# Kernel optimization log

Hardware: AMD Instinct MI355X
Metric: run time of the kernel (lower is better)

The kernel has to match this reference:

```python
import jax, jax.numpy as jnp
import numpy as np

NUM_HEADS = 16
TOP_K = 2

def setup_inputs() -> dict:
    key = jax.random.key(0)
    ks = jax.random.split(key, 5)
    B, D, E = 8192, 2048, 8
    x = jax.random.normal(ks[0], (B, D), dtype=jnp.float32)
    W_qkv = jax.random.normal(ks[1], (E, D, 3 * D), dtype=jnp.float32) * 0.02  # (in,out) per expert
    W_gate = jax.random.normal(ks[2], (D, E), dtype=jnp.float32) * 0.02
    b_gate = jnp.zeros((E,), dtype=jnp.float32)
    W_proj = jax.random.normal(ks[3], (D, D), dtype=jnp.float32) * 0.02
    b_proj = jnp.zeros((D,), dtype=jnp.float32)
    return {"x": x, "W_qkv": W_qkv, "W_gate": W_gate, "b_gate": b_gate,
            "W_proj": W_proj, "b_proj": b_proj}


def reference(x, W_qkv, W_gate, b_gate, W_proj, b_proj):
    B, D = x.shape
    E = W_qkv.shape[0]
    H = NUM_HEADS
    hd = D // H
    scale = float(hd) ** -0.5

    # gating + top-k (sparse gate weights, zeros for non-selected experts)
    gate_scores = jax.nn.softmax(x @ W_gate + b_gate, axis=-1)        # (B, E)
    topk_vals, topk_idx = jax.lax.top_k(gate_scores, TOP_K)           # (B, K)
    gw = jnp.zeros_like(gate_scores).at[jnp.arange(B)[:, None], topk_idx].add(topk_vals)

    # gate-weighted combine of expert QKV projections (linear => combine after GEMM)
    qkv = jnp.zeros((B, 3 * D), dtype=x.dtype)
    for e in range(E):  # fixed small expert count; each iter is one big GEMM
        qkv = qkv + gw[:, e:e + 1] * (x @ W_qkv[e])
    qkv = qkv.reshape(B, 3, H, hd)

    # NOTE: the torch source writes `q = k = v = torch.zeros(...)` then uses
    # in-place `+=`, so q, k, v ALIAS one tensor: all equal gate*(q_i+k_i+v_i).
    # We replicate that exact math faithfully.
    s = qkv.sum(axis=1)                                               # (B, H, hd)

    attn = jax.nn.softmax(jnp.einsum('bhd,bgd->bhg', s, s) * scale, axis=-1)  # (B, H, H)
    out = jnp.einsum('bhg,bgd->bhd', attn, s)                         # (B, H, hd)
    out = out.transpose(0, 2, 1).reshape(B, D)                        # matches .transpose(1,2).reshape
    return out @ W_proj + b_proj
```

## Files before the change

kernel.cpp:

```cpp
#include <hip/hip_runtime.h>

#define B_ROWS 8192
#define DDIM 2048
#define NEXP 8
#define NASSIGN (B_ROWS * 2)
#define MAX_TILES 80

typedef unsigned short u16;
typedef short bf16x8 __attribute__((ext_vector_type(8)));
typedef float f32x4 __attribute__((ext_vector_type(4)));

#define M_CNT 0
#define M_FILL 8
#define M_SEG 16
#define M_CTRA 24
#define M_CTRB 32
#define M_NT 40
#define M_TE 48
#define M_TB 128
#define M_TR 208

__device__ __forceinline__ u16 f2b(float f) {
  union { float f; unsigned u; } c; c.f = f;
  return (u16)((c.u + 0x7fffu + ((c.u >> 16) & 1u)) >> 16);
}
__device__ __forceinline__ float b2f(u16 h) {
  union { unsigned u; float f; } c; c.u = ((unsigned)h) << 16;
  return c.f;
}
__device__ __forceinline__ void async16(u16* lds, const u16* g) {
  __builtin_amdgcn_global_load_lds(
      (const __attribute__((address_space(1))) unsigned int*)g,
      (__attribute__((address_space(3))) unsigned int*)lds, 16, 0, 0);
}

__global__ void init_meta_kernel(int* meta) {
  int t = threadIdx.x;
  if (t < 48) meta[t] = 0;
}

template <int NSUM>
__global__ __launch_bounds__(256) void prep_transpose(
    const float* __restrict__ Win, u16* __restrict__ Wout, int ldin) {
  __shared__ u16 tl[64][72];
  int bx = blockIdx.x;
  int nt = bx & 31, kt = (bx >> 5) & 31, e = bx >> 10;
  int t = threadIdx.x;
  const size_t in_base = (size_t)e * DDIM * (size_t)ldin;
  int k0 = kt * 64, n0 = nt * 64;
#pragma unroll
  for (int i = 0; i < 4; ++i) {
    int idx = i * 256 + t;
    int kl = idx >> 4, f4 = idx & 15;
    const float* p = Win + in_base + (size_t)(k0 + kl) * ldin + n0 + f4 * 4;
    float4 v = *(const float4*)p;
    if (NSUM == 3) {
      float4 v1 = *(const float4*)(p + 2048);
      float4 v2 = *(const float4*)(p + 4096);
      v.x += v1.x + v2.x; v.y += v1.y + v2.y;
      v.z += v1.z + v2.z; v.w += v1.w + v2.w;
    }
    tl[f4 * 4 + 0][kl] = f2b(v.x);
    tl[f4 * 4 + 1][kl] = f2b(v.y);
    tl[f4 * 4 + 2][kl] = f2b(v.z);
    tl[f4 * 4 + 3][kl] = f2b(v.w);
  }
  __syncthreads();
  u16* out = Wout + (size_t)e * DDIM * DDIM;
#pragma unroll
  for (int i = 0; i < 2; ++i) {
    int idx = i * 256 + t;
    int nl = idx >> 3, kc = idx & 7;
    const u16* r = &tl[nl][kc * 8];
    uint4 pk;
    pk.x = (unsigned)r[0] | ((unsigned)r[1] << 16);
    pk.y = (unsigned)r[2] | ((unsigned)r[3] << 16);
    pk.z = (unsigned)r[4] | ((unsigned)r[5] << 16);
    pk.w = (unsigned)r[6] | ((unsigned)r[7] << 16);
    *(uint4*)(out + (size_t)(n0 + nl) * DDIM + k0 + kc * 8) = pk;
  }
}

__global__ __launch_bounds__(256) void gate_kernel(
    const float* __restrict__ x, const float* __restrict__ Wg,
    const float* __restrict__ bg, u16* __restrict__ xb,
    int* __restrict__ e01, float* __restrict__ w01, int* __restrict__ meta) {
  int b = blockIdx.x, t = threadIdx.x;
  const float* xr = x + (size_t)b * DDIM;
  float4 v0 = ((const float4*)xr)[2 * t];
  float4 v1 = ((const float4*)xr)[2 * t + 1];
  float xv[8] = {v0.x, v0.y, v0.z, v0.w, v1.x, v1.y, v1.z, v1.w};
  uint4 pk;
  pk.x = (unsigned)f2b(xv[0]) | ((unsigned)f2b(xv[1]) << 16);
  pk.y = (unsigned)f2b(xv[2]) | ((unsigned)f2b(xv[3]) << 16);
  pk.z = (unsigned)f2b(xv[4]) | ((unsigned)f2b(xv[5]) << 16);
  pk.w = (unsigned)f2b(xv[6]) | ((unsigned)f2b(xv[7]) << 16);
  *(uint4*)(xb + (size_t)b * DDIM + t * 8) = pk;

  double acc[8] = {0, 0, 0, 0, 0, 0, 0, 0};
#pragma unroll
  for (int j = 0; j < 8; ++j) {
    const float4* wr = (const float4*)(Wg + (size_t)(t * 8 + j) * 8);
    float4 wa = wr[0], wb = wr[1];
    double xd = (double)xv[j];
    acc[0] += xd * wa.x; acc[1] += xd * wa.y;
    acc[2] += xd * wa.z; acc[3] += xd * wa.w;
    acc[4] += xd * wb.x; acc[5] += xd * wb.y;
    acc[6] += xd * wb.z; acc[7] += xd * wb.w;
  }
#pragma unroll
  for (int e = 0; e < 8; ++e)
    for (int m2 = 32; m2; m2 >>= 1) acc[e] += __shfl_xor(acc[e], m2);
  __shared__ double red[4][8];
  if ((t & 63) == 0)
    for (int e = 0; e < 8; ++e) red[t >> 6][e] = acc[e];
  __syncthreads();
  if (t == 0) {
    double l[8];
    for (int e = 0; e < 8; ++e)
      l[e] = red[0][e] + red[1][e] + red[2][e] + red[3][e] + (double)bg[e];
    double mx = l[0];
    for (int e = 1; e < 8; ++e) mx = l[e] > mx ? l[e] : mx;
    double p[8], s = 0;
    for (int e = 0; e < 8; ++e) { p[e] = exp(l[e] - mx); s += p[e]; }
    int i1 = 0;
    for (int e = 1; e < 8; ++e) if (p[e] > p[i1]) i1 = e;
    int i2 = (i1 == 0) ? 1 : 0;
    for (int e = 0; e < 8; ++e)
      if (e != i1 && p[e] > p[i2]) i2 = e;
    e01[2 * b] = i1; e01[2 * b + 1] = i2;
    w01[2 * b] = (float)(p[i1] / s);
    w01[2 * b + 1] = (float)(p[i2] / s);
    atomicAdd(&meta[M_CNT + i1], 1);
    atomicAdd(&meta[M_CNT + i2], 1);
  }
}

__global__ void scan_kernel(int* meta) {
  if (threadIdx.x != 0) return;
  int total = 0;
  for (int e = 0; e < 8; ++e) { meta[M_SEG + e] = total; total += meta[M_CNT + e]; }
  int tt = 0;
  for (int e = 0; e < 8; ++e) {
    int cnt = meta[M_CNT + e];
    int ntl = (cnt + 255) >> 8;
    for (int i = 0; i < ntl; ++i) {
      meta[M_TE + tt] = e;
      meta[M_TB + tt] = meta[M_SEG + e] + i * 256;
      meta[M_TR + tt] = cnt - i * 256;
      ++tt;
    }
  }
  meta[M_NT] = tt;
  for (; tt < MAX_TILES; ++tt) { meta[M_TE + tt] = 0; meta[M_TB + tt] = 0; meta[M_TR + tt] = 0; }
}

__global__ __launch_bounds__(256) void build_kernel(
    const int* __restrict__ e01, const float* __restrict__ w01,
    int* __restrict__ meta, int* __restrict__ rows, float* __restrict__ wt,
    int* __restrict__ rowpos) {
  int b = blockIdx.x * 256 + threadIdx.x;
  if (b >= B_ROWS) return;
#pragma unroll
  for (int s = 0; s < 2; ++s) {
    int e = e01[2 * b + s];
    float w = w01[2 * b + s];
    int p = meta[M_SEG + e] + atomicAdd(&meta[M_FILL + e], 1);
    rows[p] = b;
    wt[p] = w;
    rowpos[2 * b + s] = p;
  }
}

#define BAR()                           \
  do {                                  \
    __builtin_amdgcn_sched_barrier(0);  \
    __builtin_amdgcn_s_barrier();       \
    __builtin_amdgcn_sched_barrier(0);  \
  } while (0)
#define VMCNT2() asm volatile("s_waitcnt vmcnt(2)" ::: "memory")
#define VMCNT0() asm volatile("s_waitcnt vmcnt(0)" ::: "memory")
#define LGKM0()                                       \
  do {                                                \
    asm volatile("s_waitcnt lgkmcnt(0)" ::: "memory"); \
    __builtin_amdgcn_sched_barrier(0);                \
  } while (0)

#define STAGE_A(L, T, BB) async16(&lds[BB][0][(L)*4096 + t * 8], srcA[L] + (size_t)(T)*64)
#define STAGE_B(L, T, BB) async16(&lds[BB][1][(L)*4096 + t * 8], srcB[L] + (size_t)(T)*64)

#define READ_A(QM)                                                   \
  do {                                                               \
    _Pragma("unroll") for (int i_ = 0; i_ < 4; ++i_) {               \
      int rb_ = baseA + ((QM)*64 + i_ * 16) * 128;                   \
      af[i_][0] = *(const bf16x8*)(pA + rb_ + ck0);                  \
      af[i_][1] = *(const bf16x8*)(pA + rb_ + ck1);                  \
    }                                                                \
  } while (0)
#define READ_B(H)                                                    \
  do {                                                               \
    _Pragma("unroll") for (int j_ = 0; j_ < 2; ++j_) {               \
      int rb_ = baseB + (((H)*2 + j_) * 16) * 128;                   \
      bfr[(H)*2 + j_][0] = *(const bf16x8*)(pB + rb_ + ck0);         \
      bfr[(H)*2 + j_][1] = *(const bf16x8*)(pB + rb_ + ck1);         \
    }                                                                \
  } while (0)
#define MFMA16(QM, QN)                                                         \
  do {                                                                         \
    _Pragma("unroll") for (int i_ = 0; i_ < 4; ++i_) {                         \
      _Pragma("unroll") for (int j_ = 0; j_ < 2; ++j_) {                       \
        acc[(QM)*4 + i_][(QN)*2 + j_] = __builtin_amdgcn_mfma_f32_16x16x32_bf16( \
            af[i_][0], bfr[(QN)*2 + j_][0], acc[(QM)*4 + i_][(QN)*2 + j_], 0, 0, 0); \
        acc[(QM)*4 + i_][(QN)*2 + j_] = __builtin_amdgcn_mfma_f32_16x16x32_bf16( \
            af[i_][1], bfr[(QN)*2 + j_][1], acc[(QM)*4 + i_][(QN)*2 + j_], 0, 0, 0); \
      }                                                                        \
    }                                                                          \
  } while (0)

template <int MODE>
__global__ __launch_bounds__(512, 2) void gemm256_kernel(
    const u16* __restrict__ A, const u16* __restrict__ BT,
    int* __restrict__ meta, const int* __restrict__ rows,
    const float* __restrict__ wt, const float* __restrict__ bias,
    u16* __restrict__ Yc, float* __restrict__ Out) {
  __shared__ __align__(16) u16 lds[2][2][16384];
  __shared__ int s_w;

  const int t = threadIdx.x;
  const int lane = t & 63;
  const int wid = t >> 6;
  const int wr = wid >> 2, wc = wid & 3;
  const int l15 = lane & 15;
  const int kg = lane >> 4;
  const int sw = lane & 7;
  const int baseA = (wr * 128 + l15) * 128;
  const int baseB = (wc * 64 + l15) * 128;
  const int ck0 = ((0 * 4 + kg) ^ sw) << 4;
  const int ck1 = ((1 * 4 + kg) ^ sw) << 4;

  const int nt = (MODE == 0) ? meta[M_NT] : 32;
  const int ctrbase = (MODE == 0) ? M_CTRA : M_CTRB;

  int xcd;
  asm volatile("s_getreg_b32 %0, hwreg(20, 0, 4)" : "=s"(xcd));
  xcd &= 7;

  int q = 0;

  for (;;) {
    if (t == 0) {
      int pk = -1;
      while (q < 8) {
        int qq = (xcd + q) & 7;
        int tlo_ = (qq * nt) >> 3;
        int cnt_ = (((qq + 1) * nt) >> 3) - tlo_;
        int w = atomicAdd(&meta[ctrbase + qq], 1);
        if (w < cnt_ * 8) { pk = (qq << 16) | w; break; }
        ++q;
      }
      s_w = pk;
    }
    __syncthreads();
    const int pk = s_w;
    if (pk < 0) return;
    const int qq = pk >> 16, w = pk & 0xffff;
    const int tlo = (qq * nt) >> 3;
    const int cnt = (((qq + 1) * nt) >> 3) - tlo;
    const int fp = cnt >> 1;
    int mt, n0i;
    if (w < fp * 16) {
      mt = tlo + ((w >> 4) << 1) + (w & 1);
      n0i = (w >> 1) & 7;
    } else {
      mt = tlo + cnt - 1;
      n0i = w - fp * 16;
    }
    const int n0 = n0i << 8;

    int e = 0, base = 0, rem = 256, m0 = 0;
    if (MODE == 0) {
      rem = meta[M_TR + mt];
      if (rem > 256) rem = 256;
      e = meta[M_TE + mt];
      base = meta[M_TB + mt];
    } else {
      m0 = mt << 8;
    }

    const u16* srcA[4];
    const u16* srcB[4];
#pragma unroll
    for (int L = 0; L < 4; ++L) {
      int row = L * 64 + (t >> 3);
      int cl = (t & 7) ^ (row & 7);
      int grow;
      if (MODE == 0) {
        int rl = row < rem ? row : 0;
        grow = rows[base + rl];
      } else {
        grow = m0 + row;
      }
      srcA[L] = A + (size_t)grow * DDIM + cl * 8;
      srcB[L] = BT + ((size_t)e * DDIM + n0 + row) * DDIM + cl * 8;
    }

    f32x4 acc[8][4];
#pragma unroll
    for (int i = 0; i < 8; ++i)
#pragma unroll
      for (int j = 0; j < 4; ++j) {
        f32x4 z = {0.f, 0.f, 0.f, 0.f};
        acc[i][j] = z;
      }

    bf16x8 af[4][2];
    bf16x8 bfr[4][2];

    STAGE_A(0, 0, 0); STAGE_A(1, 0, 0); STAGE_A(2, 0, 0); STAGE_A(3, 0, 0);
    STAGE_B(0, 0, 0); STAGE_B(1, 0, 0); STAGE_B(2, 0, 0); STAGE_B(3, 0, 0);
    STAGE_A(0, 1, 1); STAGE_A(1, 1, 1);
    VMCNT2();
    BAR();

    const int NT = DDIM / 64;
    for (int T = 0; T < NT; ++T) {
      const int cb = T & 1, nb = cb ^ 1;
      const char* pA = (const char*)&lds[cb][0][0];
      const char* pB = (const char*)&lds[cb][1][0];
      READ_A(0);
      READ_B(0);
      if (T + 1 < NT) { STAGE_A(2, T + 1, nb); STAGE_A(3, T + 1, nb); }
      BAR();
      LGKM0();
      __builtin_amdgcn_s_setprio(1);
      MFMA16(0, 0);
      __builtin_amdgcn_s_setprio(0);
      BAR();
      READ_B(1);
      if (T + 1 < NT) { STAGE_B(0, T + 1, nb); STAGE_B(1, T + 1, nb); }
      BAR();
      LGKM0();
      __builtin_amdgcn_s_setprio(1);
      MFMA16(0, 1);
      __builtin_amdgcn_s_setprio(0);
      BAR();
      READ_A(1);
      if (T + 1 < NT) { STAGE_B(2, T + 1, nb); STAGE_B(3, T + 1, nb); }
      BAR();
      LGKM0();
      __builtin_amdgcn_s_setprio(1);
      MFMA16(1, 0);
      __builtin_amdgcn_s_setprio(0);
      BAR();
      if (T + 2 < NT) {
        STAGE_A(0, T + 2, cb); STAGE_A(1, T + 2, cb);
        VMCNT2();
      } else {
        VMCNT0();
      }
      BAR();
      __builtin_amdgcn_s_setprio(1);
      MFMA16(1, 1);
      __builtin_amdgcn_s_setprio(0);
      BAR();
    }

    if (MODE == 1) {
      float bv[4];
#pragma unroll
      for (int fn = 0; fn < 4; ++fn) bv[fn] = bias[n0 + wc * 64 + fn * 16 + l15];
#pragma unroll
      for (int qm = 0; qm < 2; ++qm)
#pragma unroll
        for (int i = 0; i < 4; ++i)
#pragma unroll
          for (int r = 0; r < 4; ++r) {
            int rl = wr * 128 + qm * 64 + i * 16 + kg * 4 + r;
            float* orow = Out + (size_t)(m0 + rl) * DDIM + n0 + wc * 64 + l15;
#pragma unroll
            for (int fn = 0; fn < 4; ++fn)
              orow[fn * 16] = acc[qm * 4 + i][fn][r] + bv[fn];
          }
    } else {
#pragma unroll
      for (int qm = 0; qm < 2; ++qm)
#pragma unroll
        for (int i = 0; i < 4; ++i)
#pragma unroll
          for (int r = 0; r < 4; ++r) {
            int rl = wr * 128 + qm * 64 + i * 16 + kg * 4 + r;
            if (rl < rem) {
              int pos = base + rl;
              float w2 = wt[pos];
              u16* yrow = Yc + (size_t)pos * DDIM + n0 + wc * 64 + l15;
#pragma unroll
              for (int fn = 0; fn < 4; ++fn)
                yrow[fn * 16] = f2b(w2 * acc[qm * 4 + i][fn][r]);
            }
          }
    }
  }
}

__global__ __launch_bounds__(256) void combine_attn_kernel(
    const u16* __restrict__ Yc, const int* __restrict__ rowpos,
    u16* __restrict__ ab) {
  __shared__ __align__(16) float sm[16][132];
  __shared__ float at[16][17];
  __shared__ __align__(16) float osm[16][132];
  int b = blockIdx.x, t = threadIdx.x;
  int p0 = rowpos[2 * b], p1 = rowpos[2 * b + 1];
  uint4 ya = *(const uint4*)(Yc + (size_t)p0 * DDIM + t * 8);
  uint4 yb = *(const uint4*)(Yc + (size_t)p1 * DDIM + t * 8);
  const unsigned* au = (const unsigned*)&ya;
  const unsigned* bu = (const unsigned*)&yb;
  float v[8];
#pragma unroll
  for (int j = 0; j < 4; ++j) {
    v[2 * j] = b2f((u16)(au[j] & 0xffff)) + b2f((u16)(bu[j] & 0xffff));
    v[2 * j + 1] = b2f((u16)(au[j] >> 16)) + b2f((u16)(bu[j] >> 16));
  }
  {
    int row = t >> 4, col = (t & 15) * 8;
    float4 w0 = {v[0], v[1], v[2], v[3]};
    float4 w1 = {v[4], v[5], v[6], v[7]};
    *(float4*)&sm[row][col] = w0;
    *(float4*)&sm[row][col + 4] = w1;
  }
  __syncthreads();
  const int h = t >> 4, g = t & 15;
  {
    const float4* sh4 = (const float4*)&sm[h][0];
    const float4* sg4 = (const float4*)&sm[g][0];
    float4 a4 = {0.f, 0.f, 0.f, 0.f};
#pragma unroll
    for (int j = 0; j < 32; ++j) {
      float4 xa = sh4[j], xc = sg4[j];
      a4.x += xa.x * xc.x; a4.y += xa.y * xc.y;
      a4.z += xa.z * xc.z; a4.w += xa.w * xc.w;
    }
    float dot = (a4.x + a4.y) + (a4.z + a4.w);
    float lg = dot * 0.088388347648318447f;
    float mx = lg;
#pragma unroll
    for (int m2 = 8; m2; m2 >>= 1) mx = fmaxf(mx, __shfl_xor(mx, m2, 16));
    float ex = expf(lg - mx);
    float sum = ex;
#pragma unroll
    for (int m2 = 8; m2; m2 >>= 1) sum += __shfl_xor(sum, m2, 16);
    at[h][g] = ex / sum;
  }
  __syncthreads();
  {
    const int c = t & 15;
    float4 o0 = {0.f, 0.f, 0.f, 0.f};
    float4 o1 = {0.f, 0.f, 0.f, 0.f};
#pragma unroll
    for (int gg = 0; gg < 16; ++gg) {
      float w = at[h][gg];
      float4 s0 = *(const float4*)&sm[gg][c * 4];
      float4 s1 = *(const float4*)&sm[gg][64 + c * 4];
      o0.x += w * s0.x; o0.y += w * s0.y; o0.z += w * s0.z; o0.w += w * s0.w;
      o1.x += w * s1.x; o1.y += w * s1.y; o1.z += w * s1.z; o1.w += w * s1.w;
    }
    *(float4*)&osm[h][c * 4] = o0;
    *(float4*)&osm[h][64 + c * 4] = o1;
  }
  __syncthreads();
  uint4 pk;
  unsigned w2[4];
#pragma unroll
  for (int j = 0; j < 4; ++j) {
    int f0 = t * 8 + 2 * j, f1 = t * 8 + 2 * j + 1;
    w2[j] = (unsigned)f2b(osm[f0 & 15][f0 >> 4]) |
            ((unsigned)f2b(osm[f1 & 15][f1 >> 4]) << 16);
  }
  pk.x = w2[0]; pk.y = w2[1]; pk.z = w2[2]; pk.w = w2[3];
  *(uint4*)(ab + (size_t)b * DDIM + t * 8) = pk;
}

extern "C" void kernel_launch(void* const* d_in, const int* in_sizes, int n_in,
                              void* d_out, int out_size, void* d_ws, size_t ws_size,
                              hipStream_t stream) {
  const float* x = (const float*)d_in[0];
  const float* Wqkv = (const float*)d_in[1];
  const float* Wg = (const float*)d_in[2];
  const float* bg = (const float*)d_in[3];
  const float* Wp = (const float*)d_in[4];
  const float* bp = (const float*)d_in[5];
  float* out = (float*)d_out;

  char* ws = (char*)d_ws;
  size_t off = 0;
  auto alloc = [&](size_t bytes) {
    void* p = ws + off;
    off += (bytes + 255) & ~(size_t)255;
    return p;
  };
  u16* xb = (u16*)alloc((size_t)B_ROWS * DDIM * 2);
  u16* WsumT = (u16*)alloc((size_t)NEXP * DDIM * DDIM * 2);
  u16* WprojT = (u16*)alloc((size_t)DDIM * DDIM * 2);
  u16* Yc = (u16*)alloc((size_t)NASSIGN * DDIM * 2);
  u16* ab = (u16*)alloc((size_t)B_ROWS * DDIM * 2);
  int* e01 = (int*)alloc((size_t)NASSIGN * 4);
  float* w01 = (float*)alloc((size_t)NASSIGN * 4);
  int* rows = (int*)alloc((size_t)NASSIGN * 4);
  float* wt = (float*)alloc((size_t)NASSIGN * 4);
  int* rowpos = (int*)alloc((size_t)NASSIGN * 4);
  int* meta = (int*)alloc(4096);

  init_meta_kernel<<<dim3(1), dim3(64), 0, stream>>>(meta);
  prep_transpose<3><<<dim3(NEXP * 32 * 32), dim3(256), 0, stream>>>(Wqkv, WsumT, 3 * DDIM);
  prep_transpose<1><<<dim3(32 * 32), dim3(256), 0, stream>>>(Wp, WprojT, DDIM);
  gate_kernel<<<dim3(B_ROWS), dim3(256), 0, stream>>>(x, Wg, bg, xb, e01, w01, meta);
  scan_kernel<<<dim3(1), dim3(64), 0, stream>>>(meta);
  build_kernel<<<dim3(32), dim3(256), 0, stream>>>(e01, w01, meta, rows, wt, rowpos);
  gemm256_kernel<0><<<dim3(256), dim3(512), 0, stream>>>(
      xb, WsumT, meta, rows, wt, nullptr, Yc, nullptr);
  combine_attn_kernel<<<dim3(B_ROWS), dim3(256), 0, stream>>>(Yc, rowpos, ab);
  gemm256_kernel<1><<<dim3(256), dim3(512), 0, stream>>>(
      ab, WprojT, meta, rows, wt, bp, nullptr, out);
  (void)in_sizes; (void)n_in; (void)out_size; (void)ws_size;
}
```

Measured before the change: 734.0 us.

## Prefetch full tiles two steps ahead in GEMM and parallelize tile scan

The GEMM main loop now issues all A and B loads for tile T+2 into the buffer just consumed, instead of splitting T+1 loads across phases into the other buffer. The prologue loads two full tiles and the wait allows eight outstanding loads, which deepens the prefetch distance to hide global latency. The single-thread scan kernel is also parallelized across 128 threads so each tile descriptor is written by its own thread. The risk is that writing into the current buffer while other waves may still be reading it depends on barrier placement, and the load issue is bunched into fewer phases.

New measurement: 721.6 us. Within noise of the previous version (-1.7%).

```diff
diff --git a/kernel.cpp b/kernel.cpp
--- a/kernel.cpp
+++ b/kernel.cpp
@@ -136,23 +136,32 @@
   }
 }
 
-__global__ void scan_kernel(int* meta) {
-  if (threadIdx.x != 0) return;
-  int total = 0;
-  for (int e = 0; e < 8; ++e) { meta[M_SEG + e] = total; total += meta[M_CNT + e]; }
-  int tt = 0;
+__global__ __launch_bounds__(128) void scan_kernel(int* meta) {
+  __shared__ int scnt[8];
+  int t = threadIdx.x;
+  if (t < 8) scnt[t] = meta[M_CNT + t];
+  __syncthreads();
+  int seg[9], pre[9];
+  seg[0] = 0; pre[0] = 0;
+#pragma unroll
   for (int e = 0; e < 8; ++e) {
-    int cnt = meta[M_CNT + e];
-    int ntl = (cnt + 255) >> 8;
-    for (int i = 0; i < ntl; ++i) {
-      meta[M_TE + tt] = e;
-      meta[M_TB + tt] = meta[M_SEG + e] + i * 256;
-      meta[M_TR + tt] = cnt - i * 256;
-      ++tt;
-    }
-  }
-  meta[M_NT] = tt;
-  for (; tt < MAX_TILES; ++tt) { meta[M_TE + tt] = 0; meta[M_TB + tt] = 0; meta[M_TR + tt] = 0; }
+    seg[e + 1] = seg[e] + scnt[e];
+    pre[e + 1] = pre[e] + ((scnt[e] + 255) >> 8);
+  }
+  if (t < 8) meta[M_SEG + t] = seg[t];
+  if (t == 0) meta[M_NT] = pre[8];
+  if (t < MAX_TILES) {
+    if (t < pre[8]) {
+      int e = 0;
+      while (e < 7 && t >= pre[e + 1]) ++e;
+      int i = t - pre[e];
+      meta[M_TE + t] = e;
+      meta[M_TB + t] = seg[e] + i * 256;
+      meta[M_TR + t] = scnt[e] - i * 256;
+    } else {
+      meta[M_TE + t] = 0; meta[M_TB + t] = 0; meta[M_TR + t] = 0;
+    }
+  }
 }
 
 __global__ __launch_bounds__(256) void build_kernel(
@@ -178,7 +187,7 @@
     __builtin_amdgcn_s_barrier();       \
     __builtin_amdgcn_sched_barrier(0);  \
   } while (0)
-#define VMCNT2() asm volatile("s_waitcnt vmcnt(2)" ::: "memory")
+#define VMCNT8() asm volatile("s_waitcnt vmcnt(8)" ::: "memory")
 #define VMCNT0() asm volatile("s_waitcnt vmcnt(0)" ::: "memory")
 #define LGKM0()                                       \
   do {                                                \
@@ -316,20 +325,20 @@
     bf16x8 af[4][2];
     bf16x8 bfr[4][2];
 
+    STAGE_B(0, 0, 0); STAGE_B(1, 0, 0); STAGE_B(2, 0, 0); STAGE_B(3, 0, 0);
     STAGE_A(0, 0, 0); STAGE_A(1, 0, 0); STAGE_A(2, 0, 0); STAGE_A(3, 0, 0);
-    STAGE_B(0, 0, 0); STAGE_B(1, 0, 0); STAGE_B(2, 0, 0); STAGE_B(3, 0, 0);
-    STAGE_A(0, 1, 1); STAGE_A(1, 1, 1);
-    VMCNT2();
+    STAGE_B(0, 1, 1); STAGE_B(1, 1, 1); STAGE_B(2, 1, 1); STAGE_B(3, 1, 1);
+    STAGE_A(0, 1, 1); STAGE_A(1, 1, 1); STAGE_A(2, 1, 1); STAGE_A(3, 1, 1);
+    VMCNT8();
     BAR();
 
     const int NT = DDIM / 64;
     for (int T = 0; T < NT; ++T) {
-      const int cb = T & 1, nb = cb ^ 1;
+      const int cb = T & 1;
       const char* pA = (const char*)&lds[cb][0][0];
       const char* pB = (const char*)&lds[cb][1][0];
       READ_A(0);
       READ_B(0);
-      if (T + 1 < NT) { STAGE_A(2, T + 1, nb); STAGE_A(3, T + 1, nb); }
       BAR();
       LGKM0();
       __builtin_amdgcn_s_setprio(1);
@@ -337,7 +346,6 @@
       __builtin_amdgcn_s_setprio(0);
       BAR();
       READ_B(1);
-      if (T + 1 < NT) { STAGE_B(0, T + 1, nb); STAGE_B(1, T + 1, nb); }
       BAR();
       LGKM0();
       __builtin_amdgcn_s_setprio(1);
@@ -345,7 +353,10 @@
       __builtin_amdgcn_s_setprio(0);
       BAR();
       READ_A(1);
-      if (T + 1 < NT) { STAGE_B(2, T + 1, nb); STAGE_B(3, T + 1, nb); }
+      if (T + 2 < NT) {
+        STAGE_B(0, T + 2, cb); STAGE_B(1, T + 2, cb);
+        STAGE_B(2, T + 2, cb); STAGE_B(3, T + 2, cb);
+      }
       BAR();
       LGKM0();
       __builtin_amdgcn_s_setprio(1);
@@ -354,7 +365,8 @@
       BAR();
       if (T + 2 < NT) {
         STAGE_A(0, T + 2, cb); STAGE_A(1, T + 2, cb);
-        VMCNT2();
+        STAGE_A(2, T + 2, cb); STAGE_A(3, T + 2, cb);
+        VMCNT8();
       } else {
         VMCNT0();
       }
@@ -513,7 +525,7 @@
   prep_transpose<3><<<dim3(NEXP * 32 * 32), dim3(256), 0, stream>>>(Wqkv, WsumT, 3 * DDIM);
   prep_transpose<1><<<dim3(32 * 32), dim3(256), 0, stream>>>(Wp, WprojT, DDIM);
   gate_kernel<<<dim3(B_ROWS), dim3(256), 0, stream>>>(x, Wg, bg, xb, e01, w01, meta);
-  scan_kernel<<<dim3(1), dim3(64), 0, stream>>>(meta);
+  scan_kernel<<<dim3(1), dim3(128), 0, stream>>>(meta);
   build_kernel<<<dim3(32), dim3(256), 0, stream>>>(e01, w01, meta, rows, wt, rowpos);
   gemm256_kernel<0><<<dim3(256), dim3(512), 0, stream>>>(
       xb, WsumT, meta, rows, wt, nullptr, Yc, nullptr);
```
